# Kernel tuning notes

Measured on AMD Instinct MI355X. Metric: run time of the kernel, lower is better.

## Reference

```python
import jax, jax.numpy as jnp
import numpy as np

LN_EPS = 1e-5  # torch.nn.LayerNorm default


def setup_inputs() -> dict:
    key = jax.random.key(0)
    k1, k2 = jax.random.split(key)
    N, D_IN, D_OUT, G = 4096, 512, 512, 32
    x = jax.random.normal(k1, (N, D_IN), dtype=jnp.float32)
    ln_w = jnp.ones((D_IN,), dtype=jnp.float32)
    ln_b = jnp.zeros((D_IN,), dtype=jnp.float32)
    scale = 1.0 / (np.sqrt(D_IN) * np.sqrt(G))
    fouriercoeffs = jax.random.normal(k2, (2, D_OUT, D_IN, G), dtype=jnp.float32) * scale
    bias = jnp.zeros((1, D_OUT), dtype=jnp.float32)
    return {"x": x, "ln_w": ln_w, "ln_b": ln_b, "fouriercoeffs": fouriercoeffs, "bias": bias}


def reference(x, ln_w, ln_b, fouriercoeffs, bias):
    # LayerNorm over last dim
    mu = jnp.mean(x, axis=-1, keepdims=True)
    var = jnp.mean((x - mu) ** 2, axis=-1, keepdims=True)
    xn = (x - mu) * jax.lax.rsqrt(var + LN_EPS) * ln_w + ln_b
    G = fouriercoeffs.shape[-1]
    k = jnp.arange(1, G + 1, dtype=xn.dtype)           # [G]
    arg = xn[:, :, None] * k                            # [N, D_in, G]
    c = jnp.cos(arg)
    s = jnp.sin(arg)
    # contraction over (inputdim, gridsize) -> GEMM-shaped einsum
    y = jnp.einsum('big,oig->bo', c, fouriercoeffs[0])
    y = y + jnp.einsum('big,oig->bo', s, fouriercoeffs[1])
    y = y + bias
    return y
```

## Files before the change

### kernel.cpp

```cpp
#include <hip/hip_runtime.h>
#include <hip/hip_bf16.h>


#define N_ROWS 4096
#define D_IN   512
#define D_OUT  512
#define KT     16384
#define BM 128
#define BN 128
#define SPLITK 8
#define NT 64

typedef short short8 __attribute__((ext_vector_type(8)));
typedef float float4v __attribute__((ext_vector_type(4)));

__device__ inline unsigned int pack2bf(float a, float b) {
    __hip_bfloat162 h = __float22bfloat162_rn(make_float2(a, b));
    union { __hip_bfloat162 h; unsigned int u; } cv;
    cv.h = h;
    return cv.u;
}

__device__ inline unsigned short bf16_1(float a) {
    union { float f; unsigned int u; } cv;
    cv.f = a;
    unsigned int r = (cv.u + 0x7fff + ((cv.u >> 16) & 1)) >> 16;
    return (unsigned short)r;
}

__global__ __launch_bounds__(256) void pre_kernel(const float* __restrict__ x,
        const float* __restrict__ lnw, const float* __restrict__ lnb,
        const float* __restrict__ fc, float2* __restrict__ csT,
        unsigned short* __restrict__ Wb) {
    __shared__ __align__(16) float xs[16 * 516];
    __shared__ float2 murs[16];
    const int t = threadIdx.x;
    const int r0 = blockIdx.x * 16;
    {
        const int row = t >> 4, tq = t & 15;
        const float* xr = x + (size_t)(r0 + row) * D_IN;
        float s = 0.f, q = 0.f;
        #pragma unroll
        for (int k = 0; k < 8; ++k) {
            float4 v = *(const float4*)(xr + tq * 4 + k * 64);
            *(float4*)&xs[row * 516 + tq * 4 + k * 64] = v;
            s += v.x + v.y + v.z + v.w;
            q += v.x * v.x + v.y * v.y + v.z * v.z + v.w * v.w;
        }
        #pragma unroll
        for (int off = 8; off > 0; off >>= 1) {
            s += __shfl_xor(s, off, 16);
            q += __shfl_xor(q, off, 16);
        }
        if (tq == 0) {
            float mu = s * (1.f / D_IN);
            float var = q * (1.f / D_IN) - mu * mu;
            murs[row] = make_float2(mu, rsqrtf(var + 1e-5f));
        }
    }
    __syncthreads();
    {
        const int brow = t & 15, dimg = t >> 4;
        const float2 mr = murs[brow];
        #pragma unroll 4
        for (int j = 0; j < 32; ++j) {
            const int dim = j * 16 + dimg;
            float xv = xs[brow * 516 + dim];
            float xn = (xv - mr.x) * mr.y * lnw[dim] + lnb[dim];
            float s1, c1;
            __sincosf(xn, &s1, &c1);
            csT[(size_t)dim * N_ROWS + r0 + brow] = make_float2(c1, s1);
        }
    }
    {
        size_t e = ((size_t)blockIdx.x * 256 + t) * 8;
        for (int it2 = 0; it2 < 32; ++it2, e += (size_t)256 * 256 * 8) {
            const float4* in = (const float4*)(fc + e);
            float4 a = in[0], c = in[1];
            uint4 o;
            o.x = pack2bf(a.x, a.y);
            o.y = pack2bf(a.z, a.w);
            o.z = pack2bf(c.x, c.y);
            o.w = pack2bf(c.z, c.w);
            *(uint4*)(Wb + e) = o;
        }
    }
}

__device__ inline void stage_feats(unsigned short* Abuf, float2 cs, int ttype,
                                   int frow, int ihalf) {
    const float c1 = cs.x, s1 = cs.y;
    const float c2 = c1 + c1;
    float prev = ttype ? 0.f : 1.f;
    float cur  = ttype ? s1 : c1;
    const int rbase = frow * 64;
    const int sw = frow & 7;
    unsigned int us[4];
    #pragma unroll
    for (int d = 0; d < 16; ++d) {
        float f0 = cur;
        float f1 = __builtin_fmaf(c2, cur, -prev);
        float f2 = __builtin_fmaf(c2, f1, -cur);
        prev = f1;
        cur = f2;
        us[d & 3] = pack2bf(f0, f1);
        if ((d & 3) == 3) {
            const int kc = ihalf * 4 + (d >> 2);
            *(uint4*)&Abuf[rbase + ((kc ^ sw) << 3)] =
                make_uint4(us[0], us[1], us[2], us[3]);
        }
    }
}

__device__ inline void gl_lds16(const unsigned short* gsrc, unsigned short* ldst) {
    __builtin_amdgcn_global_load_lds(
        (const __attribute__((address_space(1))) unsigned int*)gsrc,
        (__attribute__((address_space(3))) unsigned int*)ldst, 16, 0, 0);
}

__device__ inline void read_af(const unsigned short* As, short8 (&af)[2][4],
                               int wm, int lm, int lq, int swA) {
    #pragma unroll
    for (int h = 0; h < 2; ++h)
        #pragma unroll
        for (int tm = 0; tm < 4; ++tm)
            af[h][tm] = *(const short8*)
                &As[(wm + tm * 16 + lm) * 64 + (((h * 4 + lq) ^ swA) << 3)];
}

__device__ inline void read_bf(const unsigned short* Bp, short8 (&bf)[2][4],
                               int bBase) {
    #pragma unroll
    for (int h = 0; h < 2; ++h)
        #pragma unroll
        for (int tn = 0; tn < 4; ++tn)
            bf[h][tn] = *(const short8*)&Bp[bBase + tn * 1024 + h * 256];
}

__device__ inline void mfma_block(short8 (&af)[2][4], short8 (&bf)[2][4],
                                  float4v (&acc)[4][4]) {
    __builtin_amdgcn_s_setprio(1);
    #pragma unroll
    for (int h = 0; h < 2; ++h)
        #pragma unroll
        for (int tm = 0; tm < 4; ++tm)
            #pragma unroll
            for (int tn = 0; tn < 4; ++tn)
                acc[tm][tn] = __builtin_amdgcn_mfma_f32_16x16x32_bf16(
                    af[h][tm], bf[h][tn], acc[tm][tn], 0, 0, 0);
    __builtin_amdgcn_s_setprio(0);
}

__global__ __launch_bounds__(256, 3) void fkan_gemm(const float2* __restrict__ csT,
        const unsigned short* __restrict__ Wb, unsigned short* __restrict__ pb) {
    __shared__ unsigned short As[BM * 64];
    __shared__ unsigned short Bs[2][BN * 64];
    const int t = threadIdx.x;
    const int row0 = blockIdx.x * BM;
    const int col0 = blockIdx.y * BN;
    const int kz = blockIdx.z;
    const int k0 = kz * 2048;
    const int i0 = kz * 64;
    const int frow = t & 127;
    const int ihalf = t >> 7;
    const int l = t & 63, wv = t >> 6;
    const int wm = (wv & 1) * 64, wn = (wv >> 1) * 64;
    const int lm = l & 15, lq = l >> 4;
    const int c8 = l & 7, s8 = l >> 3;
    const unsigned short* Bg0 = Wb + (size_t)(col0 + wv * 32 + c8) * KT + k0 + s8 * 8;
    const int swA = lm & 7;
    const int bBase = ((wn >> 3) + (lm >> 3)) * 512 + lq * 64 + (lm & 7) * 8;

    const float2* csBase = csT + (size_t)(i0 + ihalf) * N_ROWS + row0 + frow;

    float4v acc[4][4];
    #pragma unroll
    for (int i = 0; i < 4; ++i)
        #pragma unroll
        for (int j = 0; j < 4; ++j)
            acc[i][j] = (float4v){0.f, 0.f, 0.f, 0.f};

    float2 cs0 = csBase[0];
    #pragma unroll
    for (int j = 0; j < 4; ++j)
        gl_lds16(Bg0 + (size_t)(j * 8) * KT, &Bs[0][(wv * 4 + j) * 512]);
    __builtin_amdgcn_sched_barrier(0);
    float2 csA = csBase[2 * N_ROWS];
    stage_feats(As, cs0, 0, frow, ihalf);
    asm volatile("s_waitcnt vmcnt(1) lgkmcnt(0)" ::: "memory");
    __builtin_amdgcn_s_barrier();

    #pragma unroll 1
    for (int it = 0; it < NT - 1; ++it) {
        const int p = it & 1;
        short8 af[2][4];
        read_af(As, af, wm, lm, lq, swA);
        {
            const int n = it + 1;
            const unsigned short* gb =
                Bg0 + (size_t)(n >> 5) * D_OUT * KT + (n & 31) * 64;
            unsigned short* ldst = &Bs[p ^ 1][(wv * 4) * 512];
            #pragma unroll
            for (int j = 0; j < 4; ++j)
                gl_lds16(gb + (size_t)(j * 8) * KT, ldst + j * 512);
        }
        __builtin_amdgcn_sched_barrier(0);
        float2 csN = csBase[(size_t)(((it + 2) & 31) * 2) * N_ROWS];
        asm volatile("s_waitcnt lgkmcnt(0)" ::: "memory");
        __builtin_amdgcn_s_barrier();
        stage_feats(As, csA, (it + 1) >> 5, frow, ihalf);
        csA = csN;
        short8 bf[2][4];
        read_bf(&Bs[p][0], bf, bBase);
        mfma_block(af, bf, acc);
        asm volatile("s_waitcnt vmcnt(1) lgkmcnt(0)" ::: "memory");
        __builtin_amdgcn_s_barrier();
    }
    {
        short8 af[2][4];
        read_af(As, af, wm, lm, lq, swA);
        short8 bf[2][4];
        read_bf(&Bs[1][0], bf, bBase);
        mfma_block(af, bf, acc);
    }
    unsigned short* pc = pb + (size_t)kz * N_ROWS * D_OUT;
    #pragma unroll
    for (int tm = 0; tm < 4; ++tm)
        #pragma unroll
        for (int tn = 0; tn < 4; ++tn)
            #pragma unroll
            for (int r = 0; r < 4; ++r) {
                const int row = row0 + wm + tm * 16 + lq * 4 + r;
                const int col = col0 + wn + tn * 16 + lm;
                pc[(size_t)row * D_OUT + col] = bf16_1(acc[tm][tn][r]);
            }
}

__global__ __launch_bounds__(256) void reduce_kernel(const unsigned short* __restrict__ pb,
        const float* __restrict__ bias, float* __restrict__ out) {
    const size_t e = ((size_t)blockIdx.x * 256 + threadIdx.x) * 4;
    const int col = (int)(e & (D_OUT - 1));
    float4 s = *(const float4*)(bias + col);
    #pragma unroll
    for (int c = 0; c < SPLITK; ++c) {
        ushort4 u = *(const ushort4*)(pb + (size_t)c * N_ROWS * D_OUT + e);
        union { unsigned int u; float f; } f0, f1, f2, f3;
        f0.u = (unsigned int)u.x << 16;
        f1.u = (unsigned int)u.y << 16;
        f2.u = (unsigned int)u.z << 16;
        f3.u = (unsigned int)u.w << 16;
        s.x += f0.f; s.y += f1.f; s.z += f2.f; s.w += f3.f;
    }
    *(float4*)(out + e) = s;
}

extern "C" void kernel_launch(void* const* d_in, const int* in_sizes, int n_in,
                              void* d_out, int out_size, void* d_ws, size_t ws_size,
                              hipStream_t stream) {
    const float* x    = (const float*)d_in[0];
    const float* ln_w = (const float*)d_in[1];
    const float* ln_b = (const float*)d_in[2];
    const float* fc   = (const float*)d_in[3];
    const float* bias = (const float*)d_in[4];
    float* out = (float*)d_out;

    float2* csT = (float2*)d_ws;
    unsigned short* Wb = (unsigned short*)((char*)d_ws + (16u << 20));
    unsigned short* pbp = (unsigned short*)((char*)d_ws + (48u << 20));

    pre_kernel<<<256, 256, 0, stream>>>(x, ln_w, ln_b, fc, csT, Wb);
    fkan_gemm<<<dim3(N_ROWS / BM, D_OUT / BN, SPLITK), 256, 0, stream>>>(csT, Wb, pbp);
    reduce_kernel<<<2048, 256, 0, stream>>>(pbp, bias, out);
}
```

Before: 295.4 us.

## Warp-specialize GEMM into producer and consumer waves, halve split-K

```diff
diff --git a/kernel.cpp b/kernel.cpp
--- a/kernel.cpp
+++ b/kernel.cpp
@@ -8,8 +8,8 @@
 #define KT     16384
 #define BM 128
 #define BN 128
-#define SPLITK 8
-#define NT 64
+#define SPLITK 4
+#define NT 128
 
 typedef short short8 __attribute__((ext_vector_type(8)));
 typedef float float4v __attribute__((ext_vector_type(4)));
@@ -118,122 +118,112 @@
         (__attribute__((address_space(3))) unsigned int*)ldst, 16, 0, 0);
 }
 
-__device__ inline void read_af(const unsigned short* As, short8 (&af)[2][4],
-                               int wm, int lm, int lq, int swA) {
-    #pragma unroll
-    for (int h = 0; h < 2; ++h)
-        #pragma unroll
-        for (int tm = 0; tm < 4; ++tm)
-            af[h][tm] = *(const short8*)
-                &As[(wm + tm * 16 + lm) * 64 + (((h * 4 + lq) ^ swA) << 3)];
-}
-
-__device__ inline void read_bf(const unsigned short* Bp, short8 (&bf)[2][4],
-                               int bBase) {
-    #pragma unroll
-    for (int h = 0; h < 2; ++h)
-        #pragma unroll
-        for (int tn = 0; tn < 4; ++tn)
-            bf[h][tn] = *(const short8*)&Bp[bBase + tn * 1024 + h * 256];
-}
-
-__device__ inline void mfma_block(short8 (&af)[2][4], short8 (&bf)[2][4],
-                                  float4v (&acc)[4][4]) {
-    __builtin_amdgcn_s_setprio(1);
-    #pragma unroll
-    for (int h = 0; h < 2; ++h)
-        #pragma unroll
-        for (int tm = 0; tm < 4; ++tm)
-            #pragma unroll
-            for (int tn = 0; tn < 4; ++tn)
-                acc[tm][tn] = __builtin_amdgcn_mfma_f32_16x16x32_bf16(
-                    af[h][tm], bf[h][tn], acc[tm][tn], 0, 0, 0);
-    __builtin_amdgcn_s_setprio(0);
-}
-
-__global__ __launch_bounds__(256, 3) void fkan_gemm(const float2* __restrict__ csT,
+__global__ __launch_bounds__(512, 4) void fkan_gemm(const float2* __restrict__ csT,
         const unsigned short* __restrict__ Wb, unsigned short* __restrict__ pb) {
-    __shared__ unsigned short As[BM * 64];
+    __shared__ unsigned short As[2][BM * 64];
     __shared__ unsigned short Bs[2][BN * 64];
     const int t = threadIdx.x;
     const int row0 = blockIdx.x * BM;
     const int col0 = blockIdx.y * BN;
     const int kz = blockIdx.z;
-    const int k0 = kz * 2048;
-    const int i0 = kz * 64;
-    const int frow = t & 127;
-    const int ihalf = t >> 7;
-    const int l = t & 63, wv = t >> 6;
-    const int wm = (wv & 1) * 64, wn = (wv >> 1) * 64;
-    const int lm = l & 15, lq = l >> 4;
-    const int c8 = l & 7, s8 = l >> 3;
-    const unsigned short* Bg0 = Wb + (size_t)(col0 + wv * 32 + c8) * KT + k0 + s8 * 8;
-    const int swA = lm & 7;
-    const int bBase = ((wn >> 3) + (lm >> 3)) * 512 + lq * 64 + (lm & 7) * 8;
-
-    const float2* csBase = csT + (size_t)(i0 + ihalf) * N_ROWS + row0 + frow;
-
-    float4v acc[4][4];
-    #pragma unroll
-    for (int i = 0; i < 4; ++i)
+    const int k0 = kz * 4096;
+    const int i0 = kz * 128;
+
+    if (t < 256) {
+        const int l = t & 63, wv = t >> 6;
+        const int wm = (wv & 1) * 64, wn = (wv >> 1) * 64;
+        const int lm = l & 15, lq = l >> 4;
+        const int swA = lm & 7;
+        const int bBase = ((wn >> 3) + (lm >> 3)) * 512 + lq * 64 + (lm & 7) * 8;
+
+        float4v acc[4][4];
+        #pragma unroll
+        for (int i = 0; i < 4; ++i)
+            #pragma unroll
+            for (int j = 0; j < 4; ++j)
+                acc[i][j] = (float4v){0.f, 0.f, 0.f, 0.f};
+
+        __builtin_amdgcn_s_barrier();
+        asm volatile("" ::: "memory");
+        #pragma unroll 1
+        for (int it = 0; it < NT; ++it) {
+            const unsigned short* Ap = &As[it & 1][0];
+            const unsigned short* Bp = &Bs[it & 1][0];
+            __builtin_amdgcn_s_setprio(1);
+            #pragma unroll
+            for (int h = 0; h < 2; ++h) {
+                short8 af[4], bf[4];
+                #pragma unroll
+                for (int tm = 0; tm < 4; ++tm)
+                    af[tm] = *(const short8*)
+                        &Ap[(wm + tm * 16 + lm) * 64 + (((h * 4 + lq) ^ swA) << 3)];
+                #pragma unroll
+                for (int tn = 0; tn < 4; ++tn)
+                    bf[tn] = *(const short8*)&Bp[bBase + tn * 1024 + h * 256];
+                #pragma unroll
+                for (int tm = 0; tm < 4; ++tm)
+                    #pragma unroll
+                    for (int tn = 0; tn < 4; ++tn)
+                        acc[tm][tn] = __builtin_amdgcn_mfma_f32_16x16x32_bf16(
+                            af[tm], bf[tn], acc[tm][tn], 0, 0, 0);
+            }
+            __builtin_amdgcn_s_setprio(0);
+            if (it < NT - 1) {
+                asm volatile("s_waitcnt lgkmcnt(0)" ::: "memory");
+                __builtin_amdgcn_s_barrier();
+                asm volatile("" ::: "memory");
+            }
+        }
+        unsigned short* pc = pb + (size_t)kz * N_ROWS * D_OUT;
+        #pragma unroll
+        for (int tm = 0; tm < 4; ++tm)
+            #pragma unroll
+            for (int tn = 0; tn < 4; ++tn)
+                #pragma unroll
+                for (int r = 0; r < 4; ++r) {
+                    const int row = row0 + wm + tm * 16 + lq * 4 + r;
+                    const int col = col0 + wn + tn * 16 + lm;
+                    pc[(size_t)row * D_OUT + col] = bf16_1(acc[tm][tn][r]);
+                }
+    } else {
+        const int u = t - 256;
+        const int frow = u & 127;
+        const int ihalf = u >> 7;
+        const int pl = u & 63, pw = u >> 6;
+        const int c8 = pl & 7, s8 = pl >> 3;
+        const unsigned short* Bg0 =
+            Wb + (size_t)(col0 + pw * 32 + c8) * KT + k0 + s8 * 8;
+        const float2* csBase = csT + (size_t)(i0 + ihalf) * N_ROWS + row0 + frow;
+
+        float2 cs0 = csBase[0];
         #pragma unroll
         for (int j = 0; j < 4; ++j)
-            acc[i][j] = (float4v){0.f, 0.f, 0.f, 0.f};
-
-    float2 cs0 = csBase[0];
-    #pragma unroll
-    for (int j = 0; j < 4; ++j)
-        gl_lds16(Bg0 + (size_t)(j * 8) * KT, &Bs[0][(wv * 4 + j) * 512]);
-    __builtin_amdgcn_sched_barrier(0);
-    float2 csA = csBase[2 * N_ROWS];
-    stage_feats(As, cs0, 0, frow, ihalf);
-    asm volatile("s_waitcnt vmcnt(1) lgkmcnt(0)" ::: "memory");
-    __builtin_amdgcn_s_barrier();
-
-    #pragma unroll 1
-    for (int it = 0; it < NT - 1; ++it) {
-        const int p = it & 1;
-        short8 af[2][4];
-        read_af(As, af, wm, lm, lq, swA);
-        {
+            gl_lds16(Bg0 + (size_t)(j * 8) * KT, &Bs[0][(pw * 4 + j) * 512]);
+        __builtin_amdgcn_sched_barrier(0);
+        float2 csA = csBase[2 * N_ROWS];
+        stage_feats(&As[0][0], cs0, 0, frow, ihalf);
+        asm volatile("s_waitcnt vmcnt(1) lgkmcnt(0)" ::: "memory");
+        __builtin_amdgcn_s_barrier();
+        asm volatile("" ::: "memory");
+
+        #pragma unroll 1
+        for (int it = 0; it < NT - 1; ++it) {
             const int n = it + 1;
             const unsigned short* gb =
-                Bg0 + (size_t)(n >> 5) * D_OUT * KT + (n & 31) * 64;
-            unsigned short* ldst = &Bs[p ^ 1][(wv * 4) * 512];
+                Bg0 + (size_t)(n >> 6) * D_OUT * KT + (n & 63) * 64;
+            unsigned short* ldst = &Bs[n & 1][(pw * 4) * 512];
             #pragma unroll
             for (int j = 0; j < 4; ++j)
                 gl_lds16(gb + (size_t)(j * 8) * KT, ldst + j * 512);
-        }
-        __builtin_amdgcn_sched_barrier(0);
-        float2 csN = csBase[(size_t)(((it + 2) & 31) * 2) * N_ROWS];
-        asm volatile("s_waitcnt lgkmcnt(0)" ::: "memory");
-        __builtin_amdgcn_s_barrier();
-        stage_feats(As, csA, (it + 1) >> 5, frow, ihalf);
-        csA = csN;
-        short8 bf[2][4];
-        read_bf(&Bs[p][0], bf, bBase);
-        mfma_block(af, bf, acc);
-        asm volatile("s_waitcnt vmcnt(1) lgkmcnt(0)" ::: "memory");
-        __builtin_amdgcn_s_barrier();
-    }
-    {
-        short8 af[2][4];
-        read_af(As, af, wm, lm, lq, swA);
-        short8 bf[2][4];
-        read_bf(&Bs[1][0], bf, bBase);
-        mfma_block(af, bf, acc);
-    }
-    unsigned short* pc = pb + (size_t)kz * N_ROWS * D_OUT;
-    #pragma unroll
-    for (int tm = 0; tm < 4; ++tm)
-        #pragma unroll
-        for (int tn = 0; tn < 4; ++tn)
-            #pragma unroll
-            for (int r = 0; r < 4; ++r) {
-                const int row = row0 + wm + tm * 16 + lq * 4 + r;
-                const int col = col0 + wn + tn * 16 + lm;
-                pc[(size_t)row * D_OUT + col] = bf16_1(acc[tm][tn][r]);
-            }
+            __builtin_amdgcn_sched_barrier(0);
+            float2 csN = csBase[(size_t)(((it + 2) & 63) * 2) * N_ROWS];
+            stage_feats(&As[n & 1][0], csA, n >> 6, frow, ihalf);
+            csA = csN;
+            asm volatile("s_waitcnt vmcnt(1) lgkmcnt(0)" ::: "memory");
+            __builtin_amdgcn_s_barrier();
+            asm volatile("" ::: "memory");
+        }
+    }
 }
 
 __global__ __launch_bounds__(256) void reduce_kernel(const unsigned short* __restrict__ pb,
@@ -269,6 +259,6 @@
     unsigned short* pbp = (unsigned short*)((char*)d_ws + (48u << 20));
 
     pre_kernel<<<256, 256, 0, stream>>>(x, ln_w, ln_b, fc, csT, Wb);
-    fkan_gemm<<<dim3(N_ROWS / BM, D_OUT / BN, SPLITK), 256, 0, stream>>>(csT, Wb, pbp);
+    fkan_gemm<<<dim3(N_ROWS / BM, D_OUT / BN, SPLITK), 512, 0, stream>>>(csT, Wb, pbp);
     reduce_kernel<<<2048, 256, 0, stream>>>(pbp, bias, out);
 }
```

Result: faster. 265.5 us (-10.1%).

## Enlarge GEMM tile to 256x256 with 8 waves and interleaved feature staging

Applied to the files above, without the earlier changes.

```diff
diff --git a/kernel.cpp b/kernel.cpp
--- a/kernel.cpp
+++ b/kernel.cpp
@@ -6,8 +6,8 @@
 #define D_IN   512
 #define D_OUT  512
 #define KT     16384
-#define BM 128
-#define BN 128
+#define BM 256
+#define BN 256
 #define SPLITK 8
 #define NT 64
 
@@ -118,42 +118,89 @@
         (__attribute__((address_space(3))) unsigned int*)ldst, 16, 0, 0);
 }
 
-__device__ inline void read_af(const unsigned short* As, short8 (&af)[2][4],
-                               int wm, int lm, int lq, int swA) {
-    #pragma unroll
-    for (int h = 0; h < 2; ++h)
-        #pragma unroll
-        for (int tm = 0; tm < 4; ++tm)
-            af[h][tm] = *(const short8*)
-                &As[(wm + tm * 16 + lm) * 64 + (((h * 4 + lq) ^ swA) << 3)];
-}
-
-__device__ inline void read_bf(const unsigned short* Bp, short8 (&bf)[2][4],
-                               int bBase) {
-    #pragma unroll
-    for (int h = 0; h < 2; ++h)
-        #pragma unroll
-        for (int tn = 0; tn < 4; ++tn)
-            bf[h][tn] = *(const short8*)&Bp[bBase + tn * 1024 + h * 256];
-}
-
-__device__ inline void mfma_block(short8 (&af)[2][4], short8 (&bf)[2][4],
-                                  float4v (&acc)[4][4]) {
-    __builtin_amdgcn_s_setprio(1);
-    #pragma unroll
-    for (int h = 0; h < 2; ++h)
-        #pragma unroll
-        for (int tm = 0; tm < 4; ++tm)
-            #pragma unroll
-            for (int tn = 0; tn < 4; ++tn)
-                acc[tm][tn] = __builtin_amdgcn_mfma_f32_16x16x32_bf16(
-                    af[h][tm], bf[h][tn], acc[tm][tn], 0, 0, 0);
-    __builtin_amdgcn_s_setprio(0);
-}
-
-__global__ __launch_bounds__(256, 3) void fkan_gemm(const float2* __restrict__ csT,
+template<bool PF>
+__device__ __forceinline__ void gemm_tile(int tt,
+        const unsigned short* Ap, const unsigned short* Bp,
+        unsigned short* Aw, unsigned short* Bw,
+        const unsigned short* Bg0, const float2* csBase, float2& csA,
+        int wv, int wrow, int lm, int lq, int swA, int bBase,
+        int arow, int adim, float4v (&acc)[8][4]) {
+    const int ttype1 = ((tt + 1) >> 5) & 1;
+    const float c2 = csA.x + csA.x;
+    float prev = ttype1 ? 0.f : 1.f;
+    float cur  = ttype1 ? csA.y : csA.x;
+    float2 csN = csA;
+    short8 bf[2][4];
+    #pragma unroll
+    for (int p = 0; p < 4; ++p) {
+        short8 af[2][2];
+        #pragma unroll
+        for (int h = 0; h < 2; ++h)
+            #pragma unroll
+            for (int j = 0; j < 2; ++j)
+                af[h][j] = *(const short8*)
+                    &Ap[(wrow * 128 + (2 * p + j) * 16 + lm) * 64
+                        + (((h * 4 + lq) ^ swA) << 3)];
+        if (p == 0) {
+            #pragma unroll
+            for (int h = 0; h < 2; ++h)
+                #pragma unroll
+                for (int n = 0; n < 4; ++n)
+                    bf[h][n] = *(const short8*)&Bp[bBase + n * 1024 + h * 256];
+            if (PF) {
+                const int n1 = tt + 1;
+                const unsigned short* gb =
+                    Bg0 + (size_t)(n1 >> 5) * D_OUT * KT + (n1 & 31) * 64;
+                unsigned short* ldst = Bw + (wv * 4) * 512;
+                #pragma unroll
+                for (int j2 = 0; j2 < 4; ++j2)
+                    gl_lds16(gb + (size_t)(j2 * 8) * KT, ldst + j2 * 512);
+                __builtin_amdgcn_sched_barrier(0);
+                csN = csBase[(size_t)(((tt + 2) & 31) * 2) * N_ROWS];
+            }
+        }
+        if (PF) {
+            unsigned int us[4];
+            #pragma unroll
+            for (int d = 0; d < 4; ++d) {
+                float f0 = cur;
+                float f1 = __builtin_fmaf(c2, cur, -prev);
+                us[d] = pack2bf(f0, f1);
+                float f2 = __builtin_fmaf(c2, f1, -cur);
+                prev = f1;
+                cur = f2;
+            }
+            const int kc = adim * 4 + p;
+            *(uint4*)&Aw[arow * 64 + ((kc ^ (arow & 7)) << 3)] =
+                make_uint4(us[0], us[1], us[2], us[3]);
+        }
+        __builtin_amdgcn_s_barrier();
+        asm volatile("s_waitcnt lgkmcnt(0)" ::: "memory");
+        __builtin_amdgcn_s_setprio(1);
+        #pragma unroll
+        for (int h = 0; h < 2; ++h)
+            #pragma unroll
+            for (int j = 0; j < 2; ++j)
+                #pragma unroll
+                for (int n = 0; n < 4; ++n)
+                    acc[2 * p + j][n] = __builtin_amdgcn_mfma_f32_16x16x32_bf16(
+                        af[h][j], bf[h][n], acc[2 * p + j][n], 0, 0, 0);
+        __builtin_amdgcn_s_setprio(0);
+        if (p < 3) {
+            __builtin_amdgcn_s_barrier();
+            asm volatile("" ::: "memory");
+        } else if (PF) {
+            asm volatile("s_waitcnt vmcnt(1)" ::: "memory");
+            __builtin_amdgcn_s_barrier();
+            asm volatile("" ::: "memory");
+        }
+    }
+    if (PF) csA = csN;
+}
+
+__global__ __launch_bounds__(512, 2) void fkan_gemm(const float2* __restrict__ csT,
         const unsigned short* __restrict__ Wb, unsigned short* __restrict__ pb) {
-    __shared__ unsigned short As[BM * 64];
+    __shared__ unsigned short As[2][BM * 64];
     __shared__ unsigned short Bs[2][BN * 64];
     const int t = threadIdx.x;
     const int row0 = blockIdx.x * BM;
@@ -161,21 +208,20 @@
     const int kz = blockIdx.z;
     const int k0 = kz * 2048;
     const int i0 = kz * 64;
-    const int frow = t & 127;
-    const int ihalf = t >> 7;
     const int l = t & 63, wv = t >> 6;
-    const int wm = (wv & 1) * 64, wn = (wv >> 1) * 64;
+    const int wrow = wv >> 2, wcol = wv & 3;
     const int lm = l & 15, lq = l >> 4;
+    const int swA = lm & 7;
+    const int arow = t & 255, adim = t >> 8;
     const int c8 = l & 7, s8 = l >> 3;
-    const unsigned short* Bg0 = Wb + (size_t)(col0 + wv * 32 + c8) * KT + k0 + s8 * 8;
-    const int swA = lm & 7;
-    const int bBase = ((wn >> 3) + (lm >> 3)) * 512 + lq * 64 + (lm & 7) * 8;
-
-    const float2* csBase = csT + (size_t)(i0 + ihalf) * N_ROWS + row0 + frow;
-
-    float4v acc[4][4];
-    #pragma unroll
-    for (int i = 0; i < 4; ++i)
+    const unsigned short* Bg0 =
+        Wb + (size_t)(col0 + wv * 32 + c8) * KT + k0 + s8 * 8;
+    const int bBase = (wcol * 8 + (lm >> 3)) * 512 + lq * 64 + (lm & 7) * 8;
+    const float2* csBase = csT + (size_t)(i0 + adim) * N_ROWS + row0 + arow;
+
+    float4v acc[8][4];
+    #pragma unroll
+    for (int i = 0; i < 8; ++i)
         #pragma unroll
         for (int j = 0; j < 4; ++j)
             acc[i][j] = (float4v){0.f, 0.f, 0.f, 0.f};
@@ -186,53 +232,31 @@
         gl_lds16(Bg0 + (size_t)(j * 8) * KT, &Bs[0][(wv * 4 + j) * 512]);
     __builtin_amdgcn_sched_barrier(0);
     float2 csA = csBase[2 * N_ROWS];
-    stage_feats(As, cs0, 0, frow, ihalf);
+    stage_feats(&As[0][0], cs0, 0, arow, adim);
     asm volatile("s_waitcnt vmcnt(1) lgkmcnt(0)" ::: "memory");
     __builtin_amdgcn_s_barrier();
+    asm volatile("" ::: "memory");
 
     #pragma unroll 1
-    for (int it = 0; it < NT - 1; ++it) {
-        const int p = it & 1;
-        short8 af[2][4];
-        read_af(As, af, wm, lm, lq, swA);
-        {
-            const int n = it + 1;
-            const unsigned short* gb =
-                Bg0 + (size_t)(n >> 5) * D_OUT * KT + (n & 31) * 64;
-            unsigned short* ldst = &Bs[p ^ 1][(wv * 4) * 512];
-            #pragma unroll
-            for (int j = 0; j < 4; ++j)
-                gl_lds16(gb + (size_t)(j * 8) * KT, ldst + j * 512);
-        }
-        __builtin_amdgcn_sched_barrier(0);
-        float2 csN = csBase[(size_t)(((it + 2) & 31) * 2) * N_ROWS];
-        asm volatile("s_waitcnt lgkmcnt(0)" ::: "memory");
-        __builtin_amdgcn_s_barrier();
-        stage_feats(As, csA, (it + 1) >> 5, frow, ihalf);
-        csA = csN;
-        short8 bf[2][4];
-        read_bf(&Bs[p][0], bf, bBase);
-        mfma_block(af, bf, acc);
-        asm volatile("s_waitcnt vmcnt(1) lgkmcnt(0)" ::: "memory");
-        __builtin_amdgcn_s_barrier();
-    }
-    {
-        short8 af[2][4];
-        read_af(As, af, wm, lm, lq, swA);
-        short8 bf[2][4];
-        read_bf(&Bs[1][0], bf, bBase);
-        mfma_block(af, bf, acc);
-    }
+    for (int tt = 0; tt < NT - 1; ++tt)
+        gemm_tile<true>(tt, &As[tt & 1][0], &Bs[tt & 1][0],
+                        &As[(tt + 1) & 1][0], &Bs[(tt + 1) & 1][0],
+                        Bg0, csBase, csA, wv, wrow, lm, lq, swA, bBase,
+                        arow, adim, acc);
+    gemm_tile<false>(NT - 1, &As[1][0], &Bs[1][0], &As[0][0], &Bs[0][0],
+                     Bg0, csBase, csA, wv, wrow, lm, lq, swA, bBase,
+                     arow, adim, acc);
+
     unsigned short* pc = pb + (size_t)kz * N_ROWS * D_OUT;
     #pragma unroll
-    for (int tm = 0; tm < 4; ++tm)
-        #pragma unroll
-        for (int tn = 0; tn < 4; ++tn)
+    for (int m = 0; m < 8; ++m)
+        #pragma unroll
+        for (int n = 0; n < 4; ++n)
             #pragma unroll
             for (int r = 0; r < 4; ++r) {
-                const int row = row0 + wm + tm * 16 + lq * 4 + r;
-                const int col = col0 + wn + tn * 16 + lm;
-                pc[(size_t)row * D_OUT + col] = bf16_1(acc[tm][tn][r]);
+                const int row = row0 + wrow * 128 + m * 16 + lq * 4 + r;
+                const int col = col0 + wcol * 64 + n * 16 + lm;
+                pc[(size_t)row * D_OUT + col] = bf16_1(acc[m][n][r]);
             }
 }
 
@@ -269,6 +293,6 @@
     unsigned short* pbp = (unsigned short*)((char*)d_ws + (48u << 20));
 
     pre_kernel<<<256, 256, 0, stream>>>(x, ln_w, ln_b, fc, csT, Wb);
-    fkan_gemm<<<dim3(N_ROWS / BM, D_OUT / BN, SPLITK), 256, 0, stream>>>(csT, Wb, pbp);
+    fkan_gemm<<<dim3(N_ROWS / BM, D_OUT / BN, SPLITK), 512, 0, stream>>>(csT, Wb, pbp);
     reduce_kernel<<<2048, 256, 0, stream>>>(pbp, bias, out);
 }
```

Result: faster. 253.6 us (-14.2%).
